# Kernel optimization log

Measured on AMD Instinct MI355X. Metric: run time of the kernel, lower is better.

The kernel has to match this reference:

```python
import jax, jax.numpy as jnp
import numpy as np

THETA = 10000.0
N_HEADS = 16


def setup_inputs() -> dict:
    key = jax.random.key(0)
    kx, kq, kk, kv, ko = jax.random.split(key, 5)
    B, S, D = 2, 2048, 1024
    std = np.sqrt(2.0 / (D + D))
    def mk_w(k):
        # trunc_normal in [-3*std, 3*std], stored as [in_features, out_features]
        return jax.random.truncated_normal(k, -3.0, 3.0, (D, D), jnp.float32) * std
    return {
        "x": jax.random.normal(kx, (B, S, D), dtype=jnp.float32),
        "token_positions": jnp.arange(S, dtype=jnp.int64) if jax.config.jax_enable_x64 else jnp.arange(S, dtype=jnp.int32),
        "WQ": mk_w(kq),
        "WK": mk_w(kk),
        "WV": mk_w(kv),
        "WO": mk_w(ko),
    }


def _rope(x, pos, theta):
    # x: [B, H, S, d_k]; pos: [S]
    d_k = x.shape[-1]
    freq = 1.0 / theta ** (jnp.arange(0, d_k, 2, dtype=jnp.float32) / d_k)  # [d_k//2]
    ang = pos.astype(jnp.float32)[:, None] * freq                            # [S, d_k//2]
    cos, sin = jnp.cos(ang), jnp.sin(ang)
    xp = x.reshape(x.shape[:-1] + (d_k // 2, 2))
    x0, x1 = xp[..., 0], xp[..., 1]
    r0 = cos * x0 - sin * x1
    r1 = sin * x0 + cos * x1
    return jnp.stack([r0, r1], axis=-1).reshape(x.shape)


def reference(x, token_positions, WQ, WK, WV, WO):
    B, S, D = x.shape
    H = N_HEADS
    dk = D // H
    # Linear in source computes y = x @ W.T (W stored [in, out], used transposed)
    def proj(W):
        return jnp.einsum('oi,bsi->bso', W, x).reshape(B, S, H, dk).transpose(0, 2, 1, 3)
    Q = proj(WQ)  # [B, H, S, dk]
    K = proj(WK)
    V = proj(WV)
    Q = _rope(Q, token_positions, THETA)
    K = _rope(K, token_positions, THETA)
    scores = jnp.einsum('bhqd,bhkd->bhqk', Q, K) / np.sqrt(dk).astype(np.float32)
    causal = jnp.tril(jnp.ones((S, S), dtype=bool))
    scores = jnp.where(causal, scores, jnp.float32(-1e9))
    w = jax.nn.softmax(scores, axis=-1)
    out = jnp.einsum('bhqk,bhkd->bhqd', w, V)
    out = out.transpose(0, 2, 1, 3).reshape(B, S, D)
    return jnp.einsum('oi,bsi->bso', WO, out)
```

## Files before the change

kernel.cpp:

```cpp
#include <hip/hip_runtime.h>
#include <hip/hip_bf16.h>

#define S_LEN   2048
#define D_MODEL 1024
#define NH      16
#define DKH     64
#define BATCH   2
#define BS_ROWS 4096

typedef unsigned short u16;
typedef unsigned int   u32;
typedef __attribute__((ext_vector_type(4)))  float f32x4;
typedef __attribute__((ext_vector_type(16))) float f32x16;
typedef __attribute__((ext_vector_type(8)))  short bf16x8;

__device__ __forceinline__ float bf2f(u16 u) {
  union { unsigned int i; float f; } v; v.i = ((unsigned int)u) << 16; return v.f;
}
__device__ __forceinline__ u16 f2bf(float f) {
  union { __hip_bfloat16 h; u16 u; } cv; cv.h = __float2bfloat16(f); return cv.u;
}
__device__ __forceinline__ u32 pkbf(float a, float b) {
  return (u32)f2bf(a) | ((u32)f2bf(b) << 16);
}
__device__ __forceinline__ f32x4 mfma16(bf16x8 a, bf16x8 b, f32x4 c) {
  return __builtin_amdgcn_mfma_f32_16x16x32_bf16(a, b, c, 0, 0, 0);
}
__device__ __forceinline__ f32x16 mfma32(bf16x8 a, bf16x8 b, f32x16 c) {
  return __builtin_amdgcn_mfma_f32_32x32x16_bf16(a, b, c, 0, 0, 0);
}
__device__ __forceinline__ void gl_lds16(const u16* g, u16* l) {
  __builtin_amdgcn_global_load_lds(
      (const __attribute__((address_space(1))) void*)g,
      (__attribute__((address_space(3))) void*)l, 16, 0, 0);
}

__global__ void cvt_all(const float* __restrict__ x,
                        const float* __restrict__ wq, const float* __restrict__ wk,
                        const float* __restrict__ wv, const float* __restrict__ wo,
                        u16* __restrict__ xb, u16* __restrict__ wqb, u16* __restrict__ wkb,
                        u16* __restrict__ wvb, u16* __restrict__ wob) {
  int seg = blockIdx.y;
  const float* src; u16* dst;
  if (seg < 4)      { src = x + (size_t)seg * (1u << 20); dst = xb + (size_t)seg * (1u << 20); }
  else if (seg == 4){ src = wq; dst = wqb; }
  else if (seg == 5){ src = wk; dst = wkb; }
  else if (seg == 6){ src = wv; dst = wvb; }
  else              { src = wo; dst = wob; }
  int i = blockIdx.x * 256 + threadIdx.x;
  float4 v = reinterpret_cast<const float4*>(src)[i];
  ushort4 o;
  o.x = f2bf(v.x); o.y = f2bf(v.y); o.z = f2bf(v.z); o.w = f2bf(v.w);
  reinterpret_cast<ushort4*>(dst)[i] = o;
}

#define BM 128
#define BN 128
#define BKK 64

__global__ __launch_bounds__(256) void gemm_bt(
    const u16* __restrict__ A,
    const u16* __restrict__ B0, const u16* __restrict__ B1, const u16* __restrict__ B2,
    u16* __restrict__ C0, u16* __restrict__ C1, u16* __restrict__ C2,
    float* __restrict__ Cf,
    int M, int N, int K, int out_f32)
{
  __shared__ __align__(16) u16 As[BM * BKK];
  __shared__ __align__(16) u16 Bs[BN * BKK];

  const int z = blockIdx.z;
  const u16* Bm = (z == 0) ? B0 : ((z == 1) ? B1 : B2);
  u16* Cb = (z == 0) ? C0 : ((z == 1) ? C1 : C2);

  const int tid = threadIdx.x;
  const int l = tid & 63, w = tid >> 6;
  const int lr = l & 15, lg = l >> 4;
  const int m0 = blockIdx.y * BM, n0 = blockIdx.x * BN;
  const int wr = w >> 1, wc = w & 1;

  f32x4 acc[4][4];
#pragma unroll
  for (int mi = 0; mi < 4; ++mi)
#pragma unroll
    for (int nj = 0; nj < 4; ++nj)
      acc[mi][nj] = (f32x4){0.f, 0.f, 0.f, 0.f};

  for (int k0 = 0; k0 < K; k0 += BKK) {
    __syncthreads();
#pragma unroll
    for (int i = 0; i < 4; ++i) {
      int Dc = w * 256 + i * 64 + l;
      int row = Dc >> 3;
      int c = (Dc & 7) ^ (row & 7);
      gl_lds16(A  + (size_t)(m0 + row) * K + k0 + c * 8, As + (w * 256 + i * 64) * 8);
      gl_lds16(Bm + (size_t)(n0 + row) * K + k0 + c * 8, Bs + (w * 256 + i * 64) * 8);
    }
    __syncthreads();

    bf16x8 af[2][4], bfr[2][4];
#pragma unroll
    for (int kk = 0; kk < 2; ++kk)
#pragma unroll
      for (int mi = 0; mi < 4; ++mi) {
        int rowa = wr * 64 + mi * 16 + lr;
        int ck = kk * 4 + lg;
        af[kk][mi] = *(const bf16x8*)&As[rowa * BKK + (((ck) ^ (rowa & 7)) << 3)];
        int rowb = wc * 64 + mi * 16 + lr;
        bfr[kk][mi] = *(const bf16x8*)&Bs[rowb * BKK + (((ck) ^ (rowb & 7)) << 3)];
      }
#pragma unroll
    for (int kk = 0; kk < 2; ++kk)
#pragma unroll
      for (int mi = 0; mi < 4; ++mi)
#pragma unroll
        for (int nj = 0; nj < 4; ++nj)
          acc[mi][nj] = mfma16(af[kk][mi], bfr[kk][nj], acc[mi][nj]);
  }

#pragma unroll
  for (int mi = 0; mi < 4; ++mi)
#pragma unroll
    for (int nj = 0; nj < 4; ++nj)
#pragma unroll
      for (int r = 0; r < 4; ++r) {
        int row = m0 + wr * 64 + mi * 16 + lg * 4 + r;
        int col = n0 + wc * 64 + nj * 16 + lr;
        float v = acc[mi][nj][r];
        if (out_f32) Cf[(size_t)row * N + col] = v;
        else         Cb[(size_t)row * N + col] = f2bf(v);
      }
}

__global__ void rope_pack(const u16* __restrict__ Yq, const u16* __restrict__ Yk,
                          const int* __restrict__ pos,
                          u16* __restrict__ Qb, u16* __restrict__ Kb)
{
  int t = blockIdx.x * blockDim.x + threadIdx.x;
  if (t >= BS_ROWS * (D_MODEL / 2)) return;
  int pi = t & 511;
  int r  = t >> 9;
  int h = pi >> 5, j = pi & 31;
  int b = r >> 11, s = r & (S_LEN - 1);
  int p = pos[s];

  float freq = exp2f(-(float)j * 0.41524101186092028f);
  float ang = (float)p * freq;
  float sn, cs;
  sincosf(ang, &sn, &cs);

  int base = r * D_MODEL + pi * 2;
  float q0 = bf2f(Yq[base]), q1 = bf2f(Yq[base + 1]);
  float k0 = bf2f(Yk[base]), k1 = bf2f(Yk[base + 1]);

  const float QS = 0.18033688011112042f;
  float qr0 = (cs * q0 - sn * q1) * QS;
  float qr1 = (sn * q0 + cs * q1) * QS;
  float kr0 = cs * k0 - sn * k1;
  float kr1 = sn * k0 + cs * k1;

  int bh = b * NH + h;
  size_t qidx = ((size_t)bh * S_LEN + s) * DKH + 2 * j;
  ushort2 qo; qo.x = f2bf(qr0); qo.y = f2bf(qr1);
  ushort2 ko; ko.x = f2bf(kr0); ko.y = f2bf(kr1);
  *reinterpret_cast<ushort2*>(Qb + qidx) = qo;
  *reinterpret_cast<ushort2*>(Kb + qidx) = ko;
}

__global__ __launch_bounds__(256) void transpose_v(const u16* __restrict__ Yv,
                                                   u16* __restrict__ Vt)
{
  __shared__ u32 T[64][65];
  const int sb = blockIdx.x;
  const int bh = blockIdx.y;
  const int b = bh >> 4, h = bh & 15;
  const int t = threadIdx.x;
  const int s0 = sb * 64;

#pragma unroll
  for (int pass = 0; pass < 2; ++pass) {
    int row = pass * 32 + (t >> 3);
    int c0 = (t & 7) * 8;
    bf16x8 v = *(const bf16x8*)(Yv + (size_t)(b * S_LEN + s0 + row) * D_MODEL + h * DKH + c0);
#pragma unroll
    for (int i = 0; i < 8; ++i) T[row][c0 + i] = (u32)(u16)v[i];
  }
  __syncthreads();

  const int d = t >> 2, ch = t & 3;
  bf16x8 o0, o1;
#pragma unroll
  for (int i = 0; i < 8; ++i) o0[i] = (short)(u16)T[ch * 16 + i][d];
#pragma unroll
  for (int i = 0; i < 8; ++i) o1[i] = (short)(u16)T[ch * 16 + 8 + i][d];
  u16* dst = Vt + ((size_t)bh * DKH + d) * S_LEN + s0 + ch * 16;
  *(bf16x8*)dst = o0;
  *(bf16x8*)(dst + 8) = o1;
}

__global__ __launch_bounds__(64, 4) void attn_fwd(
    const u16* __restrict__ Qb, const u16* __restrict__ Kb,
    const u16* __restrict__ Vt, u16* __restrict__ Ob)
{
  const int f = blockIdx.x;
  const int qt = 63 - (f >> 5);
  const int bh = f & 31;
  const int b = bh >> 4, h = bh & 15;
  const int l = threadIdx.x & 63;
  const int lq = l & 31, hi = l >> 5;

  __shared__ __align__(16) u16 Ks[2][32 * 64];
  __shared__ __align__(16) u16 Vs[2][64 * 32];

  const u16* Qh = Qb + (size_t)bh * S_LEN * DKH;
  const u16* Kh = Kb + (size_t)bh * S_LEN * DKH;
  const u16* Vh = Vt + (size_t)bh * DKH * S_LEN;

  const int q0 = qt * 32;

  bf16x8 qf[4];
#pragma unroll
  for (int ks = 0; ks < 4; ++ks)
    qf[ks] = *(const bf16x8*)(Qh + (size_t)(q0 + lq) * DKH + ks * 16 + hi * 8);

  const u16* ksrc[4];
  const u16* vsrc[4];
#pragma unroll
  for (int i = 0; i < 4; ++i) {
    int Dc = i * 64 + l;
    int row = Dc >> 3;
    int c = (Dc & 7) ^ (row & 7);
    ksrc[i] = Kh + (size_t)row * DKH + c * 8;
  }
#pragma unroll
  for (int i = 0; i < 4; ++i) {
    int Dc = i * 64 + l;
    int d = Dc >> 2;
    int c = (Dc & 3) ^ (d & 3);
    vsrc[i] = Vh + (size_t)d * S_LEN + c * 8;
  }

  f32x16 oacc[2];
#pragma unroll
  for (int r = 0; r < 16; ++r) { oacc[0][r] = 0.f; oacc[1][r] = 0.f; }
  float lsum = 0.f;

  auto stage = [&](int buf, int t) {
    const size_t koff = (size_t)t * 32 * DKH;
    const size_t voff = (size_t)t * 32;
#pragma unroll
    for (int i = 0; i < 4; ++i) gl_lds16(ksrc[i] + koff, &Ks[buf][i * 512]);
#pragma unroll
    for (int i = 0; i < 4; ++i) gl_lds16(vsrc[i] + voff, &Vs[buf][i * 512]);
  };

  const int nt = qt + 1;
  stage(0, 0);
  int cur = 0;
  for (int t = 0; t < nt; ++t) {
    asm volatile("s_waitcnt vmcnt(4)" ::: "memory");
    __builtin_amdgcn_sched_barrier(0);
    int tn = (t + 1 < nt) ? t + 1 : nt - 1;
    stage(cur ^ 1, tn);

    f32x16 sv;
#pragma unroll
    for (int r = 0; r < 16; ++r) sv[r] = 0.f;
#pragma unroll
    for (int ks = 0; ks < 4; ++ks) {
      int c0 = ((ks * 2 + hi) ^ (lq & 7)) << 3;
      bf16x8 kf = *(const bf16x8*)&Ks[cur][lq * 64 + c0];
      sv = mfma32(kf, qf[ks], sv);
    }
    if (t == qt) {
#pragma unroll
      for (int r = 0; r < 16; ++r) {
        int kvl = (r & 3) + 8 * (r >> 2) + 4 * hi;
        if (kvl > lq) sv[r] = -1e30f;
      }
    }
    float ps = 0.f;
#pragma unroll
    for (int r = 0; r < 16; ++r) { float p = exp2f(sv[r]); sv[r] = p; ps += p; }
    lsum += ps;
    u32 w0[4], w1[4];
#pragma unroll
    for (int g = 0; g < 4; ++g) {
      w0[g] = pkbf(sv[4 * g],     sv[4 * g + 1]);
      w1[g] = pkbf(sv[4 * g + 2], sv[4 * g + 3]);
    }
    asm volatile("s_waitcnt vmcnt(8)" ::: "memory");
    __builtin_amdgcn_sched_barrier(0);
#pragma unroll
    for (int t2 = 0; t2 < 2; ++t2) {
      u32 xo0 = hi ? w0[2 * t2 + 1] : w0[2 * t2];
      u32 xo1 = hi ? w1[2 * t2 + 1] : w1[2 * t2];
      u32 sp0 = hi ? w0[2 * t2]     : w0[2 * t2 + 1];
      u32 sp1 = hi ? w1[2 * t2]     : w1[2 * t2 + 1];
      u32 yo0 = __shfl_xor(sp0, 32);
      u32 yo1 = __shfl_xor(sp1, 32);
      union { u32 u[4]; bf16x8 v; } pa;
      pa.u[0] = hi ? yo0 : xo0;
      pa.u[1] = hi ? yo1 : xo1;
      pa.u[2] = hi ? xo0 : yo0;
      pa.u[3] = hi ? xo1 : yo1;
      int cv = ((t2 * 2 + hi) ^ (lq & 3)) << 3;
#pragma unroll
      for (int dh = 0; dh < 2; ++dh) {
        bf16x8 vf = *(const bf16x8*)&Vs[cur][(dh * 32 + lq) * 32 + cv];
        oacc[dh] = mfma32(pa.v, vf, oacc[dh]);
      }
    }
    cur ^= 1;
  }

  float ltot = lsum + __shfl_xor(lsum, 32);
  float inv = 1.0f / ltot;
  u16* obase = Ob + (size_t)b * S_LEN * D_MODEL + (size_t)h * DKH;
#pragma unroll
  for (int r = 0; r < 16; ++r) {
    int ql = (r & 3) + 8 * (r >> 2) + 4 * hi;
    float ir = __shfl(inv, ql);
    u16* orow = obase + (size_t)(q0 + ql) * D_MODEL;
    orow[lq]      = f2bf(oacc[0][r] * ir);
    orow[32 + lq] = f2bf(oacc[1][r] * ir);
  }
}

extern "C" void kernel_launch(void* const* d_in, const int* in_sizes, int n_in,
                              void* d_out, int out_size, void* d_ws, size_t ws_size,
                              hipStream_t stream) {
  const float* x   = (const float*)d_in[0];
  const int*   pos = (const int*)d_in[1];
  const float* WQ  = (const float*)d_in[2];
  const float* WK  = (const float*)d_in[3];
  const float* WV  = (const float*)d_in[4];
  const float* WO  = (const float*)d_in[5];

  char* ws = (char*)d_ws;
  u16* xb  = (u16*)(ws);
  u16* wqb = (u16*)(ws + (size_t)(8)  * 1048576);
  u16* wkb = (u16*)(ws + (size_t)(10) * 1048576);
  u16* wvb = (u16*)(ws + (size_t)(12) * 1048576);
  u16* wob = (u16*)(ws + (size_t)(14) * 1048576);
  u16* Yq  = (u16*)(ws + (size_t)(16) * 1048576);
  u16* Yk  = (u16*)(ws + (size_t)(24) * 1048576);
  u16* Yv  = (u16*)(ws + (size_t)(32) * 1048576);
  u16* Qb  = (u16*)(ws + (size_t)(40) * 1048576);
  u16* Kb  = (u16*)(ws + (size_t)(48) * 1048576);
  u16* Vt  = (u16*)(ws + (size_t)(56) * 1048576);
  u16* Ob  = (u16*)(ws + (size_t)(64) * 1048576);

  cvt_all<<<dim3(1024, 8), 256, 0, stream>>>(x, WQ, WK, WV, WO, xb, wqb, wkb, wvb, wob);

  gemm_bt<<<dim3(D_MODEL / BN, BS_ROWS / BM, 3), 256, 0, stream>>>(
      xb, wqb, wkb, wvb, Yq, Yk, Yv, nullptr, BS_ROWS, D_MODEL, D_MODEL, 0);

  rope_pack<<<(BS_ROWS * (D_MODEL / 2)) / 256, 256, 0, stream>>>(
      Yq, Yk, pos, Qb, Kb);

  transpose_v<<<dim3(S_LEN / 64, BATCH * NH), 256, 0, stream>>>(Yv, Vt);

  attn_fwd<<<dim3(2048), 64, 0, stream>>>(Qb, Kb, Vt, Ob);

  gemm_bt<<<dim3(D_MODEL / BN, BS_ROWS / BM, 1), 256, 0, stream>>>(
      Ob, wob, wob, wob, nullptr, nullptr, nullptr, (float*)d_out,
      BS_ROWS, D_MODEL, D_MODEL, 1);
}
```

Before: 236.6 us.

## Split long causal attention rows across two KV chunks and combine partials

Attention work for query tiles past the midpoint is split into two KV-range chunks (split-K), each block writing unnormalized fp32 partial outputs and row sums. A new combine kernel adds the partials and normalizes into bf16. The LDS staging path is replaced with direct global-to-register loads of K and V that are double-buffered in registers, and the launch-bounds occupancy hint drops from 4 to 3. This evens out load imbalance across causal tiles. The cost is an extra kernel launch, fp32 partial traffic, and reused workspace regions (xb, Yq) that must no longer be needed at that point.

```diff
diff --git a/kernel.cpp b/kernel.cpp
--- a/kernel.cpp
+++ b/kernel.cpp
@@ -197,80 +197,58 @@
   *(bf16x8*)(dst + 8) = o1;
 }
 
-__global__ __launch_bounds__(64, 4) void attn_fwd(
+__global__ __launch_bounds__(64, 3) void attn_fwd(
     const u16* __restrict__ Qb, const u16* __restrict__ Kb,
-    const u16* __restrict__ Vt, u16* __restrict__ Ob)
-{
-  const int f = blockIdx.x;
-  const int qt = 63 - (f >> 5);
-  const int bh = f & 31;
-  const int b = bh >> 4, h = bh & 15;
+    const u16* __restrict__ Vt, float* __restrict__ Opart, float* __restrict__ lsumP)
+{
+  const int id = blockIdx.x;
+  const int c  = id >> 11;
+  const int qt = 63 - ((id >> 5) & 63);
+  if (c == 1 && qt < 32) return;
+  const int bh = (id & 7) * 4 + ((id >> 3) & 3);
   const int l = threadIdx.x & 63;
   const int lq = l & 31, hi = l >> 5;
-
-  __shared__ __align__(16) u16 Ks[2][32 * 64];
-  __shared__ __align__(16) u16 Vs[2][64 * 32];
 
   const u16* Qh = Qb + (size_t)bh * S_LEN * DKH;
   const u16* Kh = Kb + (size_t)bh * S_LEN * DKH;
   const u16* Vh = Vt + (size_t)bh * DKH * S_LEN;
 
   const int q0 = qt * 32;
+  const int t0 = c * 32;
+  const int t1 = (qt < t0 + 32) ? qt : t0 + 31;
 
   bf16x8 qf[4];
 #pragma unroll
   for (int ks = 0; ks < 4; ++ks)
     qf[ks] = *(const bf16x8*)(Qh + (size_t)(q0 + lq) * DKH + ks * 16 + hi * 8);
 
-  const u16* ksrc[4];
-  const u16* vsrc[4];
-#pragma unroll
-  for (int i = 0; i < 4; ++i) {
-    int Dc = i * 64 + l;
-    int row = Dc >> 3;
-    int c = (Dc & 7) ^ (row & 7);
-    ksrc[i] = Kh + (size_t)row * DKH + c * 8;
-  }
-#pragma unroll
-  for (int i = 0; i < 4; ++i) {
-    int Dc = i * 64 + l;
-    int d = Dc >> 2;
-    int c = (Dc & 3) ^ (d & 3);
-    vsrc[i] = Vh + (size_t)d * S_LEN + c * 8;
-  }
+  const u16* kbase = Kh + (size_t)lq * DKH + hi * 8;
+  const u16* vbase = Vh + (size_t)lq * S_LEN + hi * 8;
 
   f32x16 oacc[2];
 #pragma unroll
   for (int r = 0; r < 16; ++r) { oacc[0][r] = 0.f; oacc[1][r] = 0.f; }
   float lsum = 0.f;
 
-  auto stage = [&](int buf, int t) {
-    const size_t koff = (size_t)t * 32 * DKH;
-    const size_t voff = (size_t)t * 32;
-#pragma unroll
-    for (int i = 0; i < 4; ++i) gl_lds16(ksrc[i] + koff, &Ks[buf][i * 512]);
-#pragma unroll
-    for (int i = 0; i < 4; ++i) gl_lds16(vsrc[i] + voff, &Vs[buf][i * 512]);
+  auto LDK = [&](bf16x8 (&k)[4], int t) {
+    const u16* p = kbase + (size_t)t * (32 * DKH);
+#pragma unroll
+    for (int ks = 0; ks < 4; ++ks) k[ks] = *(const bf16x8*)(p + ks * 16);
   };
-
-  const int nt = qt + 1;
-  stage(0, 0);
-  int cur = 0;
-  for (int t = 0; t < nt; ++t) {
-    asm volatile("s_waitcnt vmcnt(4)" ::: "memory");
-    __builtin_amdgcn_sched_barrier(0);
-    int tn = (t + 1 < nt) ? t + 1 : nt - 1;
-    stage(cur ^ 1, tn);
-
+  auto LDV = [&](bf16x8 (&v)[4], int t) {
+#pragma unroll
+    for (int dh = 0; dh < 2; ++dh)
+#pragma unroll
+      for (int t2 = 0; t2 < 2; ++t2)
+        v[dh * 2 + t2] = *(const bf16x8*)(vbase + (size_t)dh * 32 * S_LEN + t * 32 + t2 * 16);
+  };
+
+  auto TILE = [&](const bf16x8 (&k)[4], const bf16x8 (&v)[4], int t) {
     f32x16 sv;
 #pragma unroll
     for (int r = 0; r < 16; ++r) sv[r] = 0.f;
 #pragma unroll
-    for (int ks = 0; ks < 4; ++ks) {
-      int c0 = ((ks * 2 + hi) ^ (lq & 7)) << 3;
-      bf16x8 kf = *(const bf16x8*)&Ks[cur][lq * 64 + c0];
-      sv = mfma32(kf, qf[ks], sv);
-    }
+    for (int ks = 0; ks < 4; ++ks) sv = mfma32(k[ks], qf[ks], sv);
     if (t == qt) {
 #pragma unroll
       for (int r = 0; r < 16; ++r) {
@@ -288,8 +266,6 @@
       w0[g] = pkbf(sv[4 * g],     sv[4 * g + 1]);
       w1[g] = pkbf(sv[4 * g + 2], sv[4 * g + 3]);
     }
-    asm volatile("s_waitcnt vmcnt(8)" ::: "memory");
-    __builtin_amdgcn_sched_barrier(0);
 #pragma unroll
     for (int t2 = 0; t2 < 2; ++t2) {
       u32 xo0 = hi ? w0[2 * t2 + 1] : w0[2 * t2];
@@ -303,26 +279,65 @@
       pa.u[1] = hi ? yo1 : xo1;
       pa.u[2] = hi ? xo0 : yo0;
       pa.u[3] = hi ? xo1 : yo1;
-      int cv = ((t2 * 2 + hi) ^ (lq & 3)) << 3;
-#pragma unroll
-      for (int dh = 0; dh < 2; ++dh) {
-        bf16x8 vf = *(const bf16x8*)&Vs[cur][(dh * 32 + lq) * 32 + cv];
-        oacc[dh] = mfma32(pa.v, vf, oacc[dh]);
-      }
-    }
-    cur ^= 1;
-  }
-
-  float ltot = lsum + __shfl_xor(lsum, 32);
-  float inv = 1.0f / ltot;
-  u16* obase = Ob + (size_t)b * S_LEN * D_MODEL + (size_t)h * DKH;
+#pragma unroll
+      for (int dh = 0; dh < 2; ++dh)
+        oacc[dh] = mfma32(pa.v, v[dh * 2 + t2], oacc[dh]);
+    }
+  };
+
+  bf16x8 kA[4], vA[4], kB[4], vB[4];
+  LDK(kA, t0); LDV(vA, t0);
+  int t = t0;
+  while (true) {
+    if (t + 1 <= t1) { LDK(kB, t + 1); LDV(vB, t + 1); }
+    TILE(kA, vA, t);
+    ++t; if (t > t1) break;
+    if (t + 1 <= t1) { LDK(kA, t + 1); LDV(vA, t + 1); }
+    TILE(kB, vB, t);
+    ++t; if (t > t1) break;
+  }
+
+  const int slot = bh * 96 + (qt < 32 ? qt : 2 * qt - 32) + c;
+  float* op = Opart + (size_t)slot * 2048;
 #pragma unroll
   for (int r = 0; r < 16; ++r) {
     int ql = (r & 3) + 8 * (r >> 2) + 4 * hi;
-    float ir = __shfl(inv, ql);
-    u16* orow = obase + (size_t)(q0 + ql) * D_MODEL;
-    orow[lq]      = f2bf(oacc[0][r] * ir);
-    orow[32 + lq] = f2bf(oacc[1][r] * ir);
+    op[ql * 64 + lq]      = oacc[0][r];
+    op[ql * 64 + 32 + lq] = oacc[1][r];
+  }
+  float lt = lsum + __shfl_xor(lsum, 32);
+  if (hi == 0) lsumP[slot * 32 + lq] = lt;
+}
+
+__global__ __launch_bounds__(64) void combine_o(const float* __restrict__ Opart,
+                                                const float* __restrict__ lsumP,
+                                                u16* __restrict__ Ob)
+{
+  const int id = blockIdx.x;
+  const int bh = id & 31, qt = id >> 5;
+  const int b = bh >> 4, h = bh & 15;
+  const int nc = (qt >> 5) + 1;
+  const int s0 = bh * 96 + (qt < 32 ? qt : 2 * qt - 32);
+  const int t = threadIdx.x;
+  const int row = t >> 1, half = t & 1;
+
+  float lsum = lsumP[s0 * 32 + row];
+  if (nc == 2) lsum += lsumP[(s0 + 1) * 32 + row];
+  const float inv = 1.0f / lsum;
+
+  const float* p0 = Opart + (size_t)s0 * 2048 + row * 64 + half * 32;
+  u16* dst = Ob + ((size_t)b * S_LEN + qt * 32 + row) * D_MODEL + h * DKH + half * 32;
+#pragma unroll
+  for (int i = 0; i < 32; i += 4) {
+    float4 v = *(const float4*)(p0 + i);
+    if (nc == 2) {
+      float4 w = *(const float4*)(p0 + 2048 + i);
+      v.x += w.x; v.y += w.y; v.z += w.z; v.w += w.w;
+    }
+    dst[i]     = f2bf(v.x * inv);
+    dst[i + 1] = f2bf(v.y * inv);
+    dst[i + 2] = f2bf(v.z * inv);
+    dst[i + 3] = f2bf(v.w * inv);
   }
 }
 
@@ -349,6 +364,8 @@
   u16* Kb  = (u16*)(ws + (size_t)(48) * 1048576);
   u16* Vt  = (u16*)(ws + (size_t)(56) * 1048576);
   u16* Ob  = (u16*)(ws + (size_t)(64) * 1048576);
+  float* Opart = (float*)(ws + (size_t)(16) * 1048576);
+  float* lsumP = (float*)(ws);
 
   cvt_all<<<dim3(1024, 8), 256, 0, stream>>>(x, WQ, WK, WV, WO, xb, wqb, wkb, wvb, wob);
 
@@ -360,7 +377,8 @@
 
   transpose_v<<<dim3(S_LEN / 64, BATCH * NH), 256, 0, stream>>>(Yv, Vt);
 
-  attn_fwd<<<dim3(2048), 64, 0, stream>>>(Qb, Kb, Vt, Ob);
+  attn_fwd<<<dim3(4096), 64, 0, stream>>>(Qb, Kb, Vt, Opart, lsumP);
+  combine_o<<<dim3(2048), 64, 0, stream>>>(Opart, lsumP, Ob);
 
   gemm_bt<<<dim3(D_MODEL / BN, BS_ROWS / BM, 1), 256, 0, stream>>>(
       Ob, wob, wob, wob, nullptr, nullptr, nullptr, (float*)d_out,
```

New measurement: 255.5 us. 8.0% more time.
